# Optimization experiments

Hardware: AMD Instinct MI355X
Metric: run time of the kernel (lower is better)

The kernel has to match this reference:

```python
import jax, jax.numpy as jnp
import numpy as np

B, S, D, H, K = 2, 4096, 256, 8, 32  # batch, seq, d_model, heads, key_dim
LN_EPS = 1e-3  # keras LayerNormalization default epsilon
NEG_INF = -1e9


def setup_inputs() -> dict:
    key = jax.random.key(0)
    ks = jax.random.split(key, 12)
    sd = 1.0 / np.sqrt(D)
    inp = {
        "x": jax.random.normal(ks[0], (B, S, D), dtype=jnp.float32),
        "Wq": jax.random.normal(ks[1], (D, H, K), dtype=jnp.float32) * sd,
        "bq": jnp.zeros((H, K), dtype=jnp.float32),
        "Wk": jax.random.normal(ks[2], (D, H, K), dtype=jnp.float32) * sd,
        "bk": jnp.zeros((H, K), dtype=jnp.float32),
        "Wv": jax.random.normal(ks[3], (D, H, K), dtype=jnp.float32) * sd,
        "bv": jnp.zeros((H, K), dtype=jnp.float32),
        "Wo": jax.random.normal(ks[4], (H, K, D), dtype=jnp.float32) * (1.0 / np.sqrt(H * K)),
        "bo": jnp.zeros((D,), dtype=jnp.float32),
        "gamma": jnp.ones((D,), dtype=jnp.float32),
        "beta": jnp.zeros((D,), dtype=jnp.float32),
        "w_2": 64,
    }
    return inp


def reference(x, Wq, bq, Wk, bk, Wv, bv, Wo, bo, gamma, beta, w_2):
    # q/k/v projections: [B,S,D] -> [B,S,H,K]
    q = jnp.einsum("bsd,dhk->bshk", x, Wq) + bq
    k = jnp.einsum("bsd,dhk->bshk", x, Wk) + bk
    v = jnp.einsum("bsd,dhk->bshk", x, Wv) + bv

    # dense scores (keras MHA computes full L^2 then masks): [B,H,S,S]
    scores = jnp.einsum("bqhk,bshk->bhqs", q, k) / jnp.sqrt(jnp.float32(K))

    # sliding-window band mask |i-j| <= w_2, applied additively like keras
    i = jnp.arange(S)
    band = (jnp.abs(i[:, None] - i[None, :]) <= w_2)  # [S,S]
    scores = scores + (1.0 - band.astype(scores.dtype)) * NEG_INF

    attn = jax.nn.softmax(scores, axis=-1)
    o = jnp.einsum("bhqs,bshk->bqhk", attn, v)
    attn_out = jnp.einsum("bqhk,hkd->bqd", o, Wo) + bo

    # residual add + LayerNorm (last axis)
    y = x + attn_out
    mu = jnp.mean(y, axis=-1, keepdims=True)
    var = jnp.mean(jnp.square(y - mu), axis=-1, keepdims=True)
    return (y - mu) * jax.lax.rsqrt(var + LN_EPS) * gamma + beta
```

## Files before the change

kernel.cpp:

```cpp
#include <hip/hip_runtime.h>
#include <hip/hip_bf16.h>
#include <cmath>

constexpr int B = 2, S = 4096, D = 256, H = 8, K = 32;
constexpr int HK = H * K;
constexpr float LN_EPS = 1e-3f;

constexpr int QT  = 64;
constexpr int WIN = 192;
constexpr int VSTRIDE = 4224;

typedef short bf16x8 __attribute__((ext_vector_type(8)));
typedef float f32x4  __attribute__((ext_vector_type(4)));

static __device__ inline short f2bf(float f) {
    unsigned u = __float_as_uint(f);
    unsigned r = (u + 0x7fffu + ((u >> 16) & 1u)) >> 16;
    return (short)r;
}

__global__ __launch_bounds__(256) void wcvt_kernel(
    const float* __restrict__ Wq, const float* __restrict__ Wk,
    const float* __restrict__ Wv, const float* __restrict__ Wo,
    const float* __restrict__ x,
    short* __restrict__ wqt, short* __restrict__ wkt,
    short* __restrict__ wvt, short* __restrict__ wot,
    short* __restrict__ vtb, short* __restrict__ xb)
{
    const int t = threadIdx.x;
    if (blockIdx.x >= 32) {
        const int i = ((blockIdx.x - 32) * 256 + t) * 8;
        const float4 a = *(const float4*)(x + i);
        const float4 b = *(const float4*)(x + i + 4);
        bf16x8 o;
        o[0] = f2bf(a.x); o[1] = f2bf(a.y); o[2] = f2bf(a.z); o[3] = f2bf(a.w);
        o[4] = f2bf(b.x); o[5] = f2bf(b.y); o[6] = f2bf(b.z); o[7] = f2bf(b.w);
        *(bf16x8*)(xb + i) = o;
        return;
    }
    const int mat = blockIdx.x >> 3, strip = blockIdx.x & 7;
    const int d0 = strip * 32;
    const float* src = (mat == 0) ? Wq : (mat == 1) ? Wk : (mat == 2) ? Wv : Wo;
    short* dst = (mat == 0) ? wqt : (mat == 1) ? wkt : (mat == 2) ? wvt : wot;

    __shared__ float lds[32][257];
    {
        const int row = t >> 3, c0 = (t & 7) * 32;
#pragma unroll
        for (int i = 0; i < 8; ++i) {
            const float4 f = *(const float4*)(src + (size_t)(d0 + row) * 256 + c0 + i * 4);
            lds[row][c0 + i * 4 + 0] = f.x; lds[row][c0 + i * 4 + 1] = f.y;
            lds[row][c0 + i * 4 + 2] = f.z; lds[row][c0 + i * 4 + 3] = f.w;
        }
    }
    __syncthreads();
    short* orow = dst + (size_t)t * 256 + d0;
#pragma unroll
    for (int u = 0; u < 4; ++u) {
        bf16x8 v;
#pragma unroll
        for (int j = 0; j < 8; ++j)
            v[j] = f2bf(lds[u * 8 + j][t]);
        *(bf16x8*)(orow + u * 8) = v;
    }

    {
        const int e0 = (blockIdx.x * 256 + t) * 8;
        const int r = e0 >> 7;
        const int c = e0 & 127;
        const int col = (c < 64) ? c : (VSTRIDE - 128 + c);
        short* p = vtb + (size_t)r * VSTRIDE + col;
#pragma unroll
        for (int j = 0; j < 8; ++j) p[j] = 0;
    }
}

__global__ __launch_bounds__(256) void qkv_gemm_kernel(
    const short* __restrict__ xb,
    const short* __restrict__ wqt, const short* __restrict__ wkt,
    const short* __restrict__ wvt,
    const float* __restrict__ bq, const float* __restrict__ bk,
    const float* __restrict__ bv,
    short* __restrict__ qb, short* __restrict__ kb, short* __restrict__ vtb)
{
    const int nt = blockIdx.x % 12, mt = blockIdx.x / 12;
    const int mat = nt >> 2, n0 = (nt & 3) * 64, m0 = mt * 128;
    const short* wt  = (mat == 0) ? wqt : (mat == 1) ? wkt : wvt;
    const float* bia = (mat == 0) ? bq  : (mat == 1) ? bk  : bv;

    const int t = threadIdx.x, wave = t >> 6, lane = t & 63;
    const int quad = lane >> 4, l16 = lane & 15;
    const int wm = wave * 32;

    const short* abase = xb + (size_t)(m0 + wm + l16) * 256 + quad * 8;
    const short* bbase = wt + (size_t)(n0 + l16) * 256 + quad * 8;

    f32x4 acc[2][4];
#pragma unroll
    for (int i = 0; i < 2; ++i)
#pragma unroll
        for (int j = 0; j < 4; ++j) acc[i][j] = (f32x4){0.f, 0.f, 0.f, 0.f};

#pragma unroll 2
    for (int k0 = 0; k0 < 256; k0 += 32) {
        bf16x8 af[2], bf[4];
#pragma unroll
        for (int mi = 0; mi < 2; ++mi)
            af[mi] = *(const bf16x8*)(abase + (size_t)mi * 16 * 256 + k0);
#pragma unroll
        for (int ni = 0; ni < 4; ++ni)
            bf[ni] = *(const bf16x8*)(bbase + (size_t)ni * 16 * 256 + k0);
#pragma unroll
        for (int mi = 0; mi < 2; ++mi)
#pragma unroll
            for (int ni = 0; ni < 4; ++ni)
                acc[mi][ni] = __builtin_amdgcn_mfma_f32_16x16x32_bf16(
                    af[mi], bf[ni], acc[mi][ni], 0, 0, 0);
    }

    if (mat < 2) {
        short* dst = (mat == 0) ? qb : kb;
#pragma unroll
        for (int ni = 0; ni < 4; ++ni) {
            const int gn = n0 + ni * 16 + l16;
            const float bb = bia[gn];
            const int h = gn >> 5, k2 = gn & 31;
#pragma unroll
            for (int mi = 0; mi < 2; ++mi)
#pragma unroll
                for (int r = 0; r < 4; ++r) {
                    const int gm = m0 + wm + mi * 16 + quad * 4 + r;
                    const int b = gm >> 12, s = gm & 4095;
                    dst[(((size_t)(b * 8 + h)) * 4096 + s) * 32 + k2] = f2bf(acc[mi][ni][r] + bb);
                }
        }
    } else {
#pragma unroll
        for (int ni = 0; ni < 4; ++ni) {
            const int gn = n0 + ni * 16 + l16;
            const float bb = bia[gn];
            const int h = gn >> 5, k2 = gn & 31;
#pragma unroll
            for (int mi = 0; mi < 2; ++mi) {
                const int gm0 = m0 + wm + mi * 16 + quad * 4;
                const int b = gm0 >> 12, s0 = gm0 & 4095;
                short4 pk;
                pk.x = f2bf(acc[mi][ni][0] + bb);
                pk.y = f2bf(acc[mi][ni][1] + bb);
                pk.z = f2bf(acc[mi][ni][2] + bb);
                pk.w = f2bf(acc[mi][ni][3] + bb);
                *(short4*)(vtb + ((size_t)(b * 8 + h) * 32 + k2) * VSTRIDE + 64 + s0) = pk;
            }
        }
    }
}

__global__ __launch_bounds__(256) void attn_kernel(
    const short* __restrict__ qb, const short* __restrict__ kb,
    const short* __restrict__ vtb, short* __restrict__ ob,
    const int* __restrict__ w2p)
{
    const int w2 = *w2p;
    const int bh   = blockIdx.x >> 6;
    const int tile = blockIdx.x & 63;
    const int i0 = tile * QT, jlo = i0 - w2;
    const int t = threadIdx.x, wave = t >> 6, lane = t & 63;
    const int quad = lane >> 4, l16 = lane & 15;

    __shared__ alignas(16) char lds[38400];
    short* Vts = (short*)lds;
    short* Ps  = (short*)(lds + 12800);

#pragma unroll
    for (int it = 0; it < 3; ++it) {
        const int idx = t + it * 256;
        const int row = idx / 24, unit = idx % 24;
        *(bf16x8*)(Vts + row * 200 + unit * 8) =
            *(const bf16x8*)(vtb + ((size_t)bh * 32 + row) * VSTRIDE + (jlo + 64) + unit * 8);
    }

    bf16x8 af[4];
#pragma unroll
    for (int mi = 0; mi < 4; ++mi)
        af[mi] = *(const bf16x8*)(qb + ((size_t)bh * 4096 + i0 + mi * 16 + l16) * 32 + quad * 8);

    f32x4 sc[4][3];
#pragma unroll
    for (int mi = 0; mi < 4; ++mi)
#pragma unroll
        for (int ni = 0; ni < 3; ++ni) sc[mi][ni] = (f32x4){0.f, 0.f, 0.f, 0.f};
#pragma unroll
    for (int ni = 0; ni < 3; ++ni) {
        const int krow = wave * 48 + ni * 16 + l16;
        const int jc = min(max(jlo + krow, 0), S - 1);
        const bf16x8 bfr = *(const bf16x8*)(kb + ((size_t)bh * 4096 + jc) * 32 + quad * 8);
#pragma unroll
        for (int mi = 0; mi < 4; ++mi)
            sc[mi][ni] = __builtin_amdgcn_mfma_f32_16x16x32_bf16(af[mi], bfr, sc[mi][ni], 0, 0, 0);
    }

    const float scale = 0.17677669529663687f;
    int colv[3]; bool jok[3];
#pragma unroll
    for (int ni = 0; ni < 3; ++ni) {
        colv[ni] = wave * 48 + ni * 16 + l16;
        const int j = jlo + colv[ni];
        jok[ni] = (j >= 0) && (j < S);
    }
    float lloc[4][4];
#pragma unroll
    for (int mi = 0; mi < 4; ++mi)
#pragma unroll
        for (int r = 0; r < 4; ++r) {
            const int row = mi * 16 + quad * 4 + r;
            float l = 0.f;
#pragma unroll
            for (int ni = 0; ni < 3; ++ni) {
                const int diff = colv[ni] - row;
                const bool valid = jok[ni] && (diff >= 0) && (diff <= 2 * w2);
                const float p = valid ? __expf(sc[mi][ni][r] * scale) : 0.f;
                l += p;
                Ps[row * 200 + colv[ni]] = f2bf(p);
            }
            lloc[mi][r] = l;
        }
#pragma unroll
    for (int mi = 0; mi < 4; ++mi)
#pragma unroll
        for (int r = 0; r < 4; ++r) {
            float l = lloc[mi][r];
#pragma unroll
            for (int off = 1; off < 16; off <<= 1)
                l += __shfl_xor(l, off);
            lloc[mi][r] = l;
        }
    if (l16 == 0) {
#pragma unroll
        for (int mi = 0; mi < 4; ++mi)
#pragma unroll
            for (int r = 0; r < 4; ++r) {
                const int row = mi * 16 + quad * 4 + r;
                ((float*)(Ps + row * 200 + 192))[wave] = lloc[mi][r];
            }
    }
    __syncthreads();

    const int orow0 = wave * 16;
    f32x4 oacc[2];
    oacc[0] = (f32x4){0.f, 0.f, 0.f, 0.f};
    oacc[1] = (f32x4){0.f, 0.f, 0.f, 0.f};
#pragma unroll
    for (int kk = 0; kk < 6; ++kk) {
        const bf16x8 pa = *(const bf16x8*)(Ps + (orow0 + l16) * 200 + kk * 32 + quad * 8);
#pragma unroll
        for (int ni = 0; ni < 2; ++ni) {
            const bf16x8 vb = *(const bf16x8*)(Vts + (ni * 16 + l16) * 200 + kk * 32 + quad * 8);
            oacc[ni] = __builtin_amdgcn_mfma_f32_16x16x32_bf16(pa, vb, oacc[ni], 0, 0, 0);
        }
    }

    const int b = bh >> 3, h = bh & 7;
#pragma unroll
    for (int r = 0; r < 4; ++r) {
        const int row = orow0 + quad * 4 + r;
        const float4 lv = *(const float4*)(Ps + row * 200 + 192);
        const float Linv = 1.f / (lv.x + lv.y + lv.z + lv.w);
        const int s = i0 + row;
#pragma unroll
        for (int ni = 0; ni < 2; ++ni) {
            const int d = ni * 16 + l16;
            ob[((size_t)b * 4096 + s) * 256 + h * 32 + d] = f2bf(oacc[ni][r] * Linv);
        }
    }
}

__global__ __launch_bounds__(256) void out_ln_kernel(
    const short* __restrict__ o, const short* __restrict__ wot,
    const float* __restrict__ x, const float* __restrict__ bo,
    const float* __restrict__ gamma, const float* __restrict__ beta,
    float* __restrict__ out)
{
    __shared__ float ys[16][260];

    const int t = threadIdx.x, wave = t >> 6, lane = t & 63;
    const int quad = lane >> 4, l16 = lane & 15;
    const int m0 = blockIdx.x * 16;
    const int wn = wave * 64;

    const short* abase = o   + (size_t)(m0 + l16) * 256 + quad * 8;
    const short* bbase = wot + (size_t)(wn + l16) * 256 + quad * 8;

    f32x4 acc[4];
#pragma unroll
    for (int j = 0; j < 4; ++j) acc[j] = (f32x4){0.f, 0.f, 0.f, 0.f};

#pragma unroll 2
    for (int k0 = 0; k0 < 256; k0 += 32) {
        const bf16x8 af = *(const bf16x8*)(abase + k0);
        bf16x8 bf[4];
#pragma unroll
        for (int ni = 0; ni < 4; ++ni)
            bf[ni] = *(const bf16x8*)(bbase + (size_t)ni * 16 * 256 + k0);
#pragma unroll
        for (int ni = 0; ni < 4; ++ni)
            acc[ni] = __builtin_amdgcn_mfma_f32_16x16x32_bf16(af, bf[ni], acc[ni], 0, 0, 0);
    }

#pragma unroll
    for (int ni = 0; ni < 4; ++ni) {
        const float bov = bo[wn + ni * 16 + l16];
#pragma unroll
        for (int r = 0; r < 4; ++r)
            ys[quad * 4 + r][wn + ni * 16 + l16] = acc[ni][r] + bov;
    }
    __syncthreads();

    const float4 g4 = *(const float4*)(gamma + lane * 4);
    const float4 b4 = *(const float4*)(beta + lane * 4);
#pragma unroll
    for (int rr = 0; rr < 4; ++rr) {
        const int row = wave * 4 + rr;
        const float4 av = *(const float4*)(&ys[row][lane * 4]);
        const float4 xv = *(const float4*)(x + (size_t)(m0 + row) * 256 + lane * 4);
        const float y0 = xv.x + av.x, y1 = xv.y + av.y, y2 = xv.z + av.z, y3 = xv.w + av.w;
        float sum = y0 + y1 + y2 + y3;
        float s2 = y0 * y0 + y1 * y1 + y2 * y2 + y3 * y3;
#pragma unroll
        for (int off = 32; off > 0; off >>= 1) {
            sum += __shfl_xor(sum, off);
            s2 += __shfl_xor(s2, off);
        }
        const float mu = sum * (1.f / 256.f);
        const float rstd = rsqrtf(s2 * (1.f / 256.f) - mu * mu + LN_EPS);
        float4 ov;
        ov.x = (y0 - mu) * rstd * g4.x + b4.x;
        ov.y = (y1 - mu) * rstd * g4.y + b4.y;
        ov.z = (y2 - mu) * rstd * g4.z + b4.z;
        ov.w = (y3 - mu) * rstd * g4.w + b4.w;
        *(float4*)(out + (size_t)(m0 + row) * 256 + lane * 4) = ov;
    }
}

extern "C" void kernel_launch(void* const* d_in, const int* in_sizes, int n_in,
                              void* d_out, int out_size, void* d_ws, size_t ws_size,
                              hipStream_t stream) {
    const float* x     = (const float*)d_in[0];
    const float* Wq    = (const float*)d_in[1];
    const float* bq    = (const float*)d_in[2];
    const float* Wk    = (const float*)d_in[3];
    const float* bk    = (const float*)d_in[4];
    const float* Wv    = (const float*)d_in[5];
    const float* bv    = (const float*)d_in[6];
    const float* Wo    = (const float*)d_in[7];
    const float* bo    = (const float*)d_in[8];
    const float* gamma = (const float*)d_in[9];
    const float* beta  = (const float*)d_in[10];
    const int*   w2p   = (const int*)d_in[11];
    float* out = (float*)d_out;

    const size_t NQ = (size_t)B * H * S * K;
    short* qb  = (short*)d_ws;
    short* kb  = qb + NQ;
    short* vtb = kb + NQ;
    short* ob  = vtb + (size_t)16 * 32 * VSTRIDE;
    short* wqt = ob + NQ;
    short* wkt = wqt + 65536;
    short* wvt = wkt + 65536;
    short* wot = wvt + 65536;
    short* xb  = wot + 65536;

    wcvt_kernel<<<dim3(32 + 1024), dim3(256), 0, stream>>>(
        Wq, Wk, Wv, Wo, x, wqt, wkt, wvt, wot, vtb, xb);

    qkv_gemm_kernel<<<dim3(768), dim3(256), 0, stream>>>(
        xb, wqt, wkt, wvt, bq, bk, bv, qb, kb, vtb);

    attn_kernel<<<dim3(B * H * S / QT), dim3(256), 0, stream>>>(
        qb, kb, vtb, ob, w2p);

    out_ln_kernel<<<dim3(B * S / 16), dim3(256), 0, stream>>>(
        ob, wot, x, bo, gamma, beta, out);
}
```

Before: 130.4 us.

## Stage QKV GEMM tiles through swizzled LDS with register prefetch

The QKV projection GEMM now stages A (x) and B (weight) tiles into shared memory with an XOR-swizzled fragment layout, instead of every wave loading its MFMA fragments straight from global memory. The block tile changes from 128x64 to 64x128 with a 2x2 wave arrangement, so each loaded element is reused across waves. The next K chunk is prefetched into registers while the current chunk is computed. The aim is to cut redundant global/L2 traffic, at the cost of LDS use, two barriers per K step, and a different launch geometry that the host launch must match.

```diff
diff --git a/kernel.cpp b/kernel.cpp
--- a/kernel.cpp
+++ b/kernel.cpp
@@ -17,6 +17,10 @@
     unsigned u = __float_as_uint(f);
     unsigned r = (u + 0x7fffu + ((u >> 16) & 1u)) >> 16;
     return (short)r;
+}
+
+static __device__ inline int frag_off(int row, int q) {
+    return ((row << 2) + (q ^ ((row >> 1) & 3))) << 4;
 }
 
 __global__ __launch_bounds__(256) void wcvt_kernel(
@@ -83,17 +87,30 @@
     const float* __restrict__ bv,
     short* __restrict__ qb, short* __restrict__ kb, short* __restrict__ vtb)
 {
-    const int nt = blockIdx.x % 12, mt = blockIdx.x / 12;
-    const int mat = nt >> 2, n0 = (nt & 3) * 64, m0 = mt * 128;
+    const int nt = blockIdx.x % 6, mt = blockIdx.x / 6;
+    const int mat = nt >> 1, n0 = (nt & 1) * 128, m0 = mt * 64;
     const short* wt  = (mat == 0) ? wqt : (mat == 1) ? wkt : wvt;
     const float* bia = (mat == 0) ? bq  : (mat == 1) ? bk  : bv;
 
+    __shared__ alignas(16) char lds[24576];
+    char* AsB = lds;
+    char* BsB = lds + 8192;
+
     const int t = threadIdx.x, wave = t >> 6, lane = t & 63;
     const int quad = lane >> 4, l16 = lane & 15;
-    const int wm = wave * 32;
-
-    const short* abase = xb + (size_t)(m0 + wm + l16) * 256 + quad * 8;
-    const short* bbase = wt + (size_t)(n0 + l16) * 256 + quad * 8;
+    const int wm = (wave & 1) * 32, wn = (wave >> 1) * 64;
+
+    int arow[2], auk[2], brow[4], buk[4];
+#pragma unroll
+    for (int i = 0; i < 2; ++i) {
+        const int idx = t * 2 + i;
+        arow[i] = idx >> 3; auk[i] = idx & 7;
+    }
+#pragma unroll
+    for (int i = 0; i < 4; ++i) {
+        const int idx = t * 4 + i;
+        brow[i] = idx >> 3; buk[i] = idx & 7;
+    }
 
     f32x4 acc[2][4];
 #pragma unroll
@@ -101,28 +118,55 @@
 #pragma unroll
         for (int j = 0; j < 4; ++j) acc[i][j] = (f32x4){0.f, 0.f, 0.f, 0.f};
 
-#pragma unroll 2
-    for (int k0 = 0; k0 < 256; k0 += 32) {
-        bf16x8 af[2], bf[4];
-#pragma unroll
-        for (int mi = 0; mi < 2; ++mi)
-            af[mi] = *(const bf16x8*)(abase + (size_t)mi * 16 * 256 + k0);
-#pragma unroll
-        for (int ni = 0; ni < 4; ++ni)
-            bf[ni] = *(const bf16x8*)(bbase + (size_t)ni * 16 * 256 + k0);
-#pragma unroll
-        for (int mi = 0; mi < 2; ++mi)
+    bf16x8 an[2], bn[4];
+#pragma unroll
+    for (int i = 0; i < 2; ++i)
+        an[i] = *(const bf16x8*)(xb + (size_t)(m0 + arow[i]) * 256 + auk[i] * 8);
+#pragma unroll
+    for (int i = 0; i < 4; ++i)
+        bn[i] = *(const bf16x8*)(wt + (size_t)(n0 + brow[i]) * 256 + buk[i] * 8);
+
+    for (int kk = 0; kk < 4; ++kk) {
+        __syncthreads();
+#pragma unroll
+        for (int i = 0; i < 2; ++i)
+            *(bf16x8*)(AsB + (auk[i] >> 2) * 4096 + frag_off(arow[i], auk[i] & 3)) = an[i];
+#pragma unroll
+        for (int i = 0; i < 4; ++i)
+            *(bf16x8*)(BsB + (buk[i] >> 2) * 8192 + frag_off(brow[i], buk[i] & 3)) = bn[i];
+        __syncthreads();
+        if (kk < 3) {
+            const int kc = (kk + 1) * 64;
+#pragma unroll
+            for (int i = 0; i < 2; ++i)
+                an[i] = *(const bf16x8*)(xb + (size_t)(m0 + arow[i]) * 256 + kc + auk[i] * 8);
+#pragma unroll
+            for (int i = 0; i < 4; ++i)
+                bn[i] = *(const bf16x8*)(wt + (size_t)(n0 + brow[i]) * 256 + kc + buk[i] * 8);
+        }
+#pragma unroll
+        for (int hh = 0; hh < 2; ++hh) {
+            bf16x8 af[2], bf[4];
+#pragma unroll
+            for (int mi = 0; mi < 2; ++mi)
+                af[mi] = *(const bf16x8*)(AsB + hh * 4096 + frag_off(wm + mi * 16 + l16, quad));
 #pragma unroll
             for (int ni = 0; ni < 4; ++ni)
-                acc[mi][ni] = __builtin_amdgcn_mfma_f32_16x16x32_bf16(
-                    af[mi], bf[ni], acc[mi][ni], 0, 0, 0);
+                bf[ni] = *(const bf16x8*)(BsB + hh * 8192 + frag_off(wn + ni * 16 + l16, quad));
+#pragma unroll
+            for (int mi = 0; mi < 2; ++mi)
+#pragma unroll
+                for (int ni = 0; ni < 4; ++ni)
+                    acc[mi][ni] = __builtin_amdgcn_mfma_f32_16x16x32_bf16(
+                        af[mi], bf[ni], acc[mi][ni], 0, 0, 0);
+        }
     }
 
     if (mat < 2) {
         short* dst = (mat == 0) ? qb : kb;
 #pragma unroll
         for (int ni = 0; ni < 4; ++ni) {
-            const int gn = n0 + ni * 16 + l16;
+            const int gn = n0 + wn + ni * 16 + l16;
             const float bb = bia[gn];
             const int h = gn >> 5, k2 = gn & 31;
 #pragma unroll
@@ -137,7 +181,7 @@
     } else {
 #pragma unroll
         for (int ni = 0; ni < 4; ++ni) {
-            const int gn = n0 + ni * 16 + l16;
+            const int gn = n0 + wn + ni * 16 + l16;
             const float bb = bia[gn];
             const int h = gn >> 5, k2 = gn & 31;
 #pragma unroll
```

Measured after the change: 119.9 us. 8.0% less time.
